# Optimization experiments

Measured on AMD Instinct MI355X. Metric: run time of the kernel, lower is better.

The kernel has to match this reference:

```python
import jax, jax.numpy as jnp
import numpy as np

DROPOUT_P = 0.5
INV_SCALE = 1.0
_DROP_KEY = jax.random.key(42)


def setup_inputs() -> dict:
    key = jax.random.key(0)
    kq, kk, kv = jax.random.split(key, 3)
    B, H, S, D = 4, 16, 2048, 64
    return {
        "query": jax.random.normal(kq, (B, H, S, D), dtype=jnp.float32),
        "key": jax.random.normal(kk, (B, H, S, D), dtype=jnp.float32),
        "value": jax.random.normal(kv, (B, H, S, D), dtype=jnp.float32),
    }


def reference(query, key, value):
    # qk = Q @ K^T, scaled, softmax over last axis
    qk = jnp.einsum("bhqd,bhkd->bhqk", query, key) / INV_SCALE
    p = jax.nn.softmax(qk, axis=-1)
    # inverted dropout with a fixed RNG key (deterministic reference)
    keep = jax.random.bernoulli(_DROP_KEY, 1.0 - DROPOUT_P, p.shape)
    p = jnp.where(keep, p / (1.0 - DROPOUT_P), 0.0)
    # attention output: P @ V
    return jnp.einsum("bhqk,bhkd->bhqd", p, value)
```

## Files before the change

kernel.cpp:

```cpp
#include <hip/hip_runtime.h>


#define S_LEN 2048
#define D_DIM 64
#define KT    32
#define QT    16
#define NWAVE 4
#define KSTR  72
#define VROW  66
#define PSTR  40

typedef short  short8  __attribute__((ext_vector_type(8)));
typedef float  floatx4 __attribute__((ext_vector_type(4)));

__device__ __forceinline__ unsigned rotl(unsigned x, int r) {
  return __builtin_amdgcn_alignbit(x, x, 32 - r);
}

__device__ __forceinline__ unsigned drop_mask(unsigned i) {
  const unsigned KS1 = 42u;
  const unsigned KS2 = 0x1BD11BDAu ^ 42u;
  unsigned a = 0u;
  unsigned b = i + KS1;
#define TFR(r) { a += b; b = rotl(b, r); b ^= a; }
  TFR(13) TFR(15) TFR(26) TFR(6)   a += KS1; b += KS2 + 1u;
  TFR(17) TFR(29) TFR(16) TFR(24)  a += KS2; b += 2u;
  TFR(13) TFR(15) TFR(26) TFR(6)             b += KS1 + 3u;
  TFR(17) TFR(29) TFR(16) TFR(24)  a += KS1; b += KS2 + 4u;
  TFR(13) TFR(15) TFR(26) TFR(6)   a += KS2; b += 5u;
#undef TFR
  return (unsigned)(((int)(a ^ b)) >> 31);
}

__device__ __forceinline__ void split_bf16(float x, unsigned short& h, unsigned short& l) {
  unsigned u = __float_as_uint(x);
  h = (unsigned short)(u >> 16);
  float r = x - __uint_as_float(u & 0xFFFF0000u);
  l = (unsigned short)(__float_as_uint(r) >> 16);
}

#define MFMA(a, b, c) __builtin_amdgcn_mfma_f32_16x16x32_bf16((a), (b), (c), 0, 0, 0)

__global__ __launch_bounds__(256)
__attribute__((amdgpu_waves_per_eu(4, 4)))
void attn_fused_v8(
    const float* __restrict__ Qg, const float* __restrict__ Kg,
    const float* __restrict__ Vg, float* __restrict__ Og) {

  __shared__ __attribute__((aligned(16))) unsigned short Kh[KT * KSTR];
  __shared__ __attribute__((aligned(16))) unsigned short Kl[KT * KSTR];
  __shared__ __attribute__((aligned(16))) unsigned short Vs[KT * VROW];
  __shared__ __attribute__((aligned(16))) unsigned short Ph[NWAVE][QT * PSTR];

  const int tid  = threadIdx.x;
  const int wave = tid >> 6;
  const int lane = tid & 63;
  const int m16  = lane & 15;
  const int quad = lane >> 4;

  const int bh    = blockIdx.x >> 5;
  const int qtile = blockIdx.x & 31;
  const int q0    = qtile * (QT * NWAVE) + wave * QT;
  const size_t head_off = (size_t)bh * S_LEN * D_DIM;

  short8 qh[2], ql[2];
#pragma unroll
  for (int kc = 0; kc < 2; ++kc) {
    const float* qp = Qg + head_off + (size_t)(q0 + m16) * D_DIM + kc * 32 + quad * 8;
    floatx4 f0 = *(const floatx4*)qp;
    floatx4 f1 = *(const floatx4*)(qp + 4);
#pragma unroll
    for (int e = 0; e < 4; ++e) {
      unsigned short h, l;
      split_bf16(f0[e], h, l);
      qh[kc][e] = (short)h;  ql[kc][e] = (short)l;
      split_bf16(f1[e], h, l);
      qh[kc][4 + e] = (short)h;  ql[kc][4 + e] = (short)l;
    }
  }

  floatx4 o_acc[4];
#pragma unroll
  for (int n = 0; n < 4; ++n) o_acc[n] = (floatx4){0.f, 0.f, 0.f, 0.f};
  float lsum[4];
#pragma unroll
  for (int r = 0; r < 4; ++r) lsum[r] = 0.f;

  const unsigned ibase0 =
      ((unsigned)(bh * S_LEN + q0 + quad * 4)) * (unsigned)S_LEN + (unsigned)m16;

  const int srow = tid >> 4;
  const int sc4  = (tid & 15) << 2;
  const float* kbase = Kg + head_off + (size_t)srow * D_DIM + sc4;
  const float* vbase = Vg + head_off + (size_t)srow * D_DIM + sc4;

  floatx4 kpre0 = *(const floatx4*)(kbase);
  floatx4 kpre1 = *(const floatx4*)(kbase + 16 * D_DIM);
  floatx4 vpre0 = *(const floatx4*)(vbase);
  floatx4 vpre1 = *(const floatx4*)(vbase + 16 * D_DIM);

  for (int kb = 0; kb < S_LEN; kb += KT) {
    asm volatile("s_waitcnt lgkmcnt(0)" ::: "memory");
    __builtin_amdgcn_s_barrier();

#pragma unroll
    for (int half = 0; half < 2; ++half) {
      floatx4 kv = half ? kpre1 : kpre0;
      floatx4 vv = half ? vpre1 : vpre0;
      int row = srow + half * 16;
      unsigned short h0, h1, h2, h3, l0, l1, l2, l3;
      split_bf16(kv[0], h0, l0); split_bf16(kv[1], h1, l1);
      split_bf16(kv[2], h2, l2); split_bf16(kv[3], h3, l3);
      int kidx = row * KSTR + sc4;
      *(unsigned*)&Kh[kidx]     = (unsigned)h0 | ((unsigned)h1 << 16);
      *(unsigned*)&Kh[kidx + 2] = (unsigned)h2 | ((unsigned)h3 << 16);
      *(unsigned*)&Kl[kidx]     = (unsigned)l0 | ((unsigned)l1 << 16);
      *(unsigned*)&Kl[kidx + 2] = (unsigned)l2 | ((unsigned)l3 << 16);
      unsigned v01 = (__float_as_uint(vv[0]) >> 16) |
                     (__float_as_uint(vv[1]) & 0xFFFF0000u);
      unsigned v23 = (__float_as_uint(vv[2]) >> 16) |
                     (__float_as_uint(vv[3]) & 0xFFFF0000u);
      int vidx = row * VROW + sc4;
      *(unsigned*)&Vs[vidx]     = v01;
      *(unsigned*)&Vs[vidx + 2] = v23;
    }

    if (kb + KT < S_LEN) {
      const float* kp = kbase + (size_t)(kb + KT) * D_DIM;
      const float* vp = vbase + (size_t)(kb + KT) * D_DIM;
      kpre0 = *(const floatx4*)(kp);
      kpre1 = *(const floatx4*)(kp + 16 * D_DIM);
      vpre0 = *(const floatx4*)(vp);
      vpre1 = *(const floatx4*)(vp + 16 * D_DIM);
    }

    asm volatile("s_waitcnt lgkmcnt(0)" ::: "memory");
    __builtin_amdgcn_s_barrier();

    floatx4 sc[2];
#pragma unroll
    for (int nb = 0; nb < 2; ++nb) {
      floatx4 acc = (floatx4){0.f, 0.f, 0.f, 0.f};
#pragma unroll
      for (int kc = 0; kc < 2; ++kc) {
        int bidx = (nb * 16 + m16) * KSTR + kc * 32 + quad * 8;
        short8 kbh = *(const short8*)&Kh[bidx];
        short8 kbl = *(const short8*)&Kl[bidx];
        acc = MFMA(qh[kc], kbh, acc);
        acc = MFMA(qh[kc], kbl, acc);
        acc = MFMA(ql[kc], kbh, acc);
      }
      sc[nb] = acc;
    }

#pragma unroll
    for (int nb = 0; nb < 2; ++nb)
#pragma unroll
      for (int r = 0; r < 4; ++r) {
        float pe = __expf(sc[nb][r]);
        lsum[r] += pe;
        unsigned i = ibase0 + (unsigned)kb + (unsigned)(r * S_LEN) + (unsigned)(nb * 16);
        unsigned hbits = (__float_as_uint(pe) >> 16) & ~drop_mask(i);
        Ph[wave][(quad * 4 + r) * PSTR + nb * 16 + m16] = (unsigned short)hbits;
      }

    short8 pa = *(const short8*)&Ph[wave][m16 * PSTR + quad * 8];
#pragma unroll
    for (int n = 0; n < 4; ++n) {
      short8 vb;
#pragma unroll
      for (int j = 0; j < 8; ++j)
        vb[j] = (short)Vs[(quad * 8 + j) * VROW + n * 16 + m16];
      o_acc[n] = MFMA(pa, vb, o_acc[n]);
    }
  }

#pragma unroll
  for (int off = 8; off >= 1; off >>= 1)
#pragma unroll
    for (int r = 0; r < 4; ++r)
      lsum[r] += __shfl_xor(lsum[r], off, 64);

#pragma unroll
  for (int r = 0; r < 4; ++r) {
    float scale = 2.0f / lsum[r];
#pragma unroll
    for (int n = 0; n < 4; ++n) {
      Og[head_off + (size_t)(q0 + quad * 4 + r) * D_DIM + n * 16 + m16] =
          o_acc[n][r] * scale;
    }
  }
}

extern "C" void kernel_launch(void* const* d_in, const int* in_sizes, int n_in,
                              void* d_out, int out_size, void* d_ws, size_t ws_size,
                              hipStream_t stream) {
  (void)in_sizes; (void)n_in; (void)out_size; (void)d_ws; (void)ws_size;
  const float* Q = (const float*)d_in[0];
  const float* K = (const float*)d_in[1];
  const float* V = (const float*)d_in[2];
  float* O = (float*)d_out;
  hipLaunchKernelGGL(attn_fused_v8, dim3(2048), dim3(256), 0, stream, Q, K, V, O);
}
```

Before: 856.7 us.

## Precompute dropout mask into workspace bitmask via separate kernel

Adds a maskgen kernel that evaluates the Threefry dropout hash once per element and packs the bits into a 32-bit-per-word mask in the workspace. The attention kernel then loads one mask word per row per key tile instead of running the hash inline. It also relaxes waves_per_eu to allow up to 8. The hash work moves into a mask-generation pass that is still timed, and the change adds 32 MB of mask writes and reads plus a second kernel launch. When no workspace is available it falls back to the inline hash.

```diff
diff --git a/kernel.cpp b/kernel.cpp
--- a/kernel.cpp
+++ b/kernel.cpp
@@ -9,6 +9,7 @@
 #define KSTR  72
 #define VROW  66
 #define PSTR  40
+#define MROW  (S_LEN / 32)
 
 typedef short  short8  __attribute__((ext_vector_type(8)));
 typedef float  floatx4 __attribute__((ext_vector_type(4)));
@@ -32,6 +33,18 @@
   return (unsigned)(((int)(a ^ b)) >> 31);
 }
 
+__global__ __launch_bounds__(512) void maskgen(unsigned* __restrict__ Mg,
+                                               unsigned n_words) {
+  unsigned wid = blockIdx.x * 512u + threadIdx.x;
+  if (wid >= n_words) return;
+  unsigned base = wid << 5;
+  unsigned w = 0u;
+#pragma unroll
+  for (int j = 0; j < 32; ++j)
+    w |= drop_mask(base + (unsigned)j) & (1u << j);
+  Mg[wid] = w;
+}
+
 __device__ __forceinline__ void split_bf16(float x, unsigned short& h, unsigned short& l) {
   unsigned u = __float_as_uint(x);
   h = (unsigned short)(u >> 16);
@@ -41,11 +54,13 @@
 
 #define MFMA(a, b, c) __builtin_amdgcn_mfma_f32_16x16x32_bf16((a), (b), (c), 0, 0, 0)
 
+template <bool USE_MASK>
 __global__ __launch_bounds__(256)
-__attribute__((amdgpu_waves_per_eu(4, 4)))
-void attn_fused_v8(
+__attribute__((amdgpu_waves_per_eu(4, 8)))
+void attn_fused(
     const float* __restrict__ Qg, const float* __restrict__ Kg,
-    const float* __restrict__ Vg, float* __restrict__ Og) {
+    const float* __restrict__ Vg, float* __restrict__ Og,
+    const unsigned* __restrict__ Mask) {
 
   __shared__ __attribute__((aligned(16))) unsigned short Kh[KT * KSTR];
   __shared__ __attribute__((aligned(16))) unsigned short Kl[KT * KSTR];
@@ -88,6 +103,7 @@
 
   const unsigned ibase0 =
       ((unsigned)(bh * S_LEN + q0 + quad * 4)) * (unsigned)S_LEN + (unsigned)m16;
+  const unsigned mbase = (unsigned)(bh * S_LEN + q0 + quad * 4) * (unsigned)MROW;
 
   const int srow = tid >> 4;
   const int sc4  = (tid & 15) << 2;
@@ -102,6 +118,13 @@
   for (int kb = 0; kb < S_LEN; kb += KT) {
     asm volatile("s_waitcnt lgkmcnt(0)" ::: "memory");
     __builtin_amdgcn_s_barrier();
+
+    unsigned mw[4] = {0u, 0u, 0u, 0u};
+    if constexpr (USE_MASK) {
+#pragma unroll
+      for (int r = 0; r < 4; ++r)
+        mw[r] = Mask[mbase + (unsigned)(r * MROW) + (unsigned)(kb >> 5)];
+    }
 
 #pragma unroll
     for (int half = 0; half < 2; ++half) {
@@ -159,8 +182,14 @@
       for (int r = 0; r < 4; ++r) {
         float pe = __expf(sc[nb][r]);
         lsum[r] += pe;
-        unsigned i = ibase0 + (unsigned)kb + (unsigned)(r * S_LEN) + (unsigned)(nb * 16);
-        unsigned hbits = (__float_as_uint(pe) >> 16) & ~drop_mask(i);
+        unsigned hbits = __float_as_uint(pe) >> 16;
+        if constexpr (USE_MASK) {
+          unsigned dm = (unsigned)(((int)(mw[r] << (31 - nb * 16 - m16))) >> 31);
+          hbits &= ~dm;
+        } else {
+          unsigned i = ibase0 + (unsigned)kb + (unsigned)(r * S_LEN) + (unsigned)(nb * 16);
+          hbits &= ~drop_mask(i);
+        }
         Ph[wave][(quad * 4 + r) * PSTR + nb * 16 + m16] = (unsigned short)hbits;
       }
 
@@ -195,10 +224,21 @@
 extern "C" void kernel_launch(void* const* d_in, const int* in_sizes, int n_in,
                               void* d_out, int out_size, void* d_ws, size_t ws_size,
                               hipStream_t stream) {
-  (void)in_sizes; (void)n_in; (void)out_size; (void)d_ws; (void)ws_size;
+  (void)in_sizes; (void)n_in; (void)out_size;
   const float* Q = (const float*)d_in[0];
   const float* K = (const float*)d_in[1];
   const float* V = (const float*)d_in[2];
   float* O = (float*)d_out;
-  hipLaunchKernelGGL(attn_fused_v8, dim3(2048), dim3(256), 0, stream, Q, K, V, O);
-}
+
+  const size_t MASK_WORDS = (size_t)64 * S_LEN * MROW;
+  if (d_ws != nullptr && ws_size >= MASK_WORDS * sizeof(unsigned)) {
+    unsigned* M = (unsigned*)d_ws;
+    hipLaunchKernelGGL(maskgen, dim3((unsigned)((MASK_WORDS + 511) / 512)),
+                       dim3(512), 0, stream, M, (unsigned)MASK_WORDS);
+    hipLaunchKernelGGL((attn_fused<true>), dim3(2048), dim3(256), 0, stream,
+                       Q, K, V, O, (const unsigned*)M);
+  } else {
+    hipLaunchKernelGGL((attn_fused<false>), dim3(2048), dim3(256), 0, stream,
+                       Q, K, V, O, (const unsigned*)nullptr);
+  }
+}
```

Result: faster. 796.5 us (-7.0%).
